# Kernel tuning notes

Measured on AMD Instinct MI355X. Metric: run time of the kernel, lower is better.

Reference implementation:

```python
import jax, jax.numpy as jnp
import numpy as np

N_EMBD = 2048
N_HEAD = 16
N_KV_HEAD = 4
HD = N_EMBD // N_HEAD  # 128
B, T = 1, 4096
EPS = 1e-6


def apply_rope(x, cos, sin):
    # x: [B,T,H,hd]; cos/sin: [T,1,hd//2]
    hd = x.shape[-1] // 2
    x1, x2 = x[..., :hd], x[..., hd:]
    y1 = x1 * cos + x2 * sin
    y2 = x2 * cos - x1 * sin
    return jnp.concatenate((y1, y2), axis=-1).astype(x.dtype)


def rms_norm(x, eps=EPS):
    return x * jax.lax.rsqrt(jnp.mean(jnp.square(x), axis=-1, keepdims=True) + eps)


def setup_inputs() -> dict:
    key = jax.random.key(0)
    ks = jax.random.split(key, 7)
    s = 0.02
    return {
        "x": jax.random.normal(ks[0], (B, T, N_EMBD), dtype=jnp.float32),
        "cos": jax.random.normal(ks[1], (T, 1, HD // 2), dtype=jnp.float32),
        "sin": jax.random.normal(ks[2], (T, 1, HD // 2), dtype=jnp.float32),
        "wq": jax.random.normal(ks[3], (N_EMBD, N_HEAD * HD), dtype=jnp.float32) * s,
        "wk": jax.random.normal(ks[4], (N_EMBD, N_KV_HEAD * HD), dtype=jnp.float32) * s,
        "wv": jax.random.normal(ks[5], (N_EMBD, N_KV_HEAD * HD), dtype=jnp.float32) * s,
        "wo": jax.random.normal(ks[6], (N_EMBD, N_EMBD), dtype=jnp.float32) * s,
    }


def reference(x, cos, sin, wq, wk, wv, wo):
    Bb, Tt, C = x.shape
    q = (x @ wq).reshape(Bb, Tt, N_HEAD, HD)
    k = (x @ wk).reshape(Bb, Tt, N_KV_HEAD, HD)
    v = (x @ wv).reshape(Bb, Tt, N_KV_HEAD, HD)
    q = rms_norm(apply_rope(q, cos, sin))
    k = rms_norm(apply_rope(k, cos, sin))
    g = N_HEAD // N_KV_HEAD
    if g > 1:
        k = jnp.repeat(k, g, axis=2)  # [B,T,H,hd]
        v = jnp.repeat(v, g, axis=2)
    scale = 1.0 / jnp.sqrt(jnp.float32(HD))
    # scores: [B,H,T,S]
    scores = jnp.einsum("bthd,bshd->bhts", q, k) * scale
    causal = jnp.tril(jnp.ones((Tt, Tt), dtype=bool))
    scores = jnp.where(causal, scores, jnp.finfo(scores.dtype).min)
    attn = jax.nn.softmax(scores, axis=-1)
    y = jnp.einsum("bhts,bshd->bthd", attn, v).reshape(Bb, Tt, C)
    return y @ wo
```

## Files before the change

### kernel.cpp

```cpp
#include <hip/hip_runtime.h>

#define T_SEQ 4096
#define C_EMB 2048
#define NH 16
#define NKV 4
#define HD 128

typedef short bf16x8 __attribute__((ext_vector_type(8)));
typedef float f32x4 __attribute__((ext_vector_type(4)));
typedef unsigned short u16x4 __attribute__((ext_vector_type(4)));

__device__ inline unsigned short f2bf(float f) {
    unsigned int u = __float_as_uint(f);
    unsigned int r = (u + 0x7FFFu + ((u >> 16) & 1u)) >> 16;
    return (unsigned short)r;
}

__device__ __forceinline__ void async_cp16(const unsigned short* g, unsigned short* l) {
    __builtin_amdgcn_global_load_lds((const __attribute__((address_space(1))) unsigned int*)g,
                                     (__attribute__((address_space(3))) unsigned int*)l,
                                     16, 0, 0);
}

__global__ __launch_bounds__(256) void cvt_bf16(const float* __restrict__ in,
                                                unsigned short* __restrict__ out, int n) {
    int i = (blockIdx.x * 256 + threadIdx.x) * 4;
    if (i >= n) return;
    float4 f = *(const float4*)(&in[i]);
    u16x4 o;
    o.x = f2bf(f.x); o.y = f2bf(f.y); o.z = f2bf(f.z); o.w = f2bf(f.w);
    *(u16x4*)(&out[i]) = o;
}

__global__ __launch_bounds__(256) void transpose_all(const float* __restrict__ wq,
                                                     const float* __restrict__ wk,
                                                     const float* __restrict__ wv,
                                                     const float* __restrict__ wo,
                                                     unsigned short* __restrict__ wqkvT,
                                                     unsigned short* __restrict__ woT) {
    __shared__ float tile[32][33];
    int z = blockIdx.z;
    const float* in;
    unsigned short* out;
    int ld_in;
    if (z == 0)      { in = wq; out = wqkvT;                         ld_in = 2048; }
    else if (z == 1) { in = wk; out = wqkvT + (size_t)2048 * 2048;   ld_in = 512;  }
    else if (z == 2) { in = wv; out = wqkvT + (size_t)2560 * 2048;   ld_in = 512;  }
    else             { in = wo; out = woT;                           ld_in = 2048; }
    if ((z == 1 || z == 2) && blockIdx.x >= 16) return;

    int x = blockIdx.x * 32 + threadIdx.x;
    for (int i = threadIdx.y; i < 32; i += 8) {
        int y = blockIdx.y * 32 + i;
        tile[i][threadIdx.x] = in[(size_t)y * ld_in + x];
    }
    __syncthreads();
    int xo = blockIdx.y * 32 + threadIdx.x;
    for (int i = threadIdx.y; i < 32; i += 8) {
        int yo = blockIdx.x * 32 + i;
        out[(size_t)yo * 2048 + xo] = f2bf(tile[threadIdx.x][i]);
    }
}

__global__ __launch_bounds__(256, 4) void gemm_qkv(const unsigned short* __restrict__ A,
                                                   const unsigned short* __restrict__ Bt,
                                                   const float* __restrict__ cosb,
                                                   const float* __restrict__ sinb,
                                                   unsigned short* __restrict__ Qn,
                                                   unsigned short* __restrict__ Kn,
                                                   unsigned short* __restrict__ Vt) {
    __shared__ __align__(16) unsigned short As[2][128 * 32];
    __shared__ __align__(16) unsigned short Bs[2][128 * 32];
    const int K = 2048;
    int t = threadIdx.x;
    int w = t >> 6, lane = t & 63;
    int ln = lane & 15, q = lane >> 4;
    int wm = w * 32;
    int m0 = blockIdx.y * 128, n0 = blockIdx.x * 128;

    f32x4 acc[2][8] = {};

#pragma unroll
    for (int s = 0; s < 2; ++s) {
        int L = s * 256 + t;
        int r = L >> 2;
        int c = (L & 3) ^ ((L >> 4) & 3);
        async_cp16(&A[(size_t)(m0 + r) * K + c * 8], &As[0][s * 2048 + w * 512]);
        async_cp16(&Bt[(size_t)(n0 + r) * K + c * 8], &Bs[0][s * 2048 + w * 512]);
    }

    for (int it = 0; it < 64; ++it) {
        __syncthreads();
        if (it < 63) {
            int k0 = (it + 1) * 32;
            int p = (it + 1) & 1;
#pragma unroll
            for (int s = 0; s < 2; ++s) {
                int L = s * 256 + t;
                int r = L >> 2;
                int c = (L & 3) ^ ((L >> 4) & 3);
                async_cp16(&A[(size_t)(m0 + r) * K + k0 + c * 8], &As[p][s * 2048 + w * 512]);
                async_cp16(&Bt[(size_t)(n0 + r) * K + k0 + c * 8], &Bs[p][s * 2048 + w * 512]);
            }
        }
        int p = it & 1;
        int cs = (q ^ ((ln >> 2) & 3)) * 8;
        bf16x8 af[2], bfr[8];
#pragma unroll
        for (int i = 0; i < 2; ++i) af[i] = *(const bf16x8*)(&As[p][(wm + i * 16 + ln) * 32 + cs]);
#pragma unroll
        for (int j = 0; j < 8; ++j) bfr[j] = *(const bf16x8*)(&Bs[p][(j * 16 + ln) * 32 + cs]);
#pragma unroll
        for (int i = 0; i < 2; ++i)
#pragma unroll
            for (int j = 0; j < 8; ++j)
                acc[i][j] = __builtin_amdgcn_mfma_f32_16x16x32_bf16(af[i], bfr[j], acc[i][j], 0, 0, 0);
    }

    if (n0 < 2560) {
        bool isQ = (n0 < 2048);
        int h = isQ ? (n0 >> 7) : ((n0 - 2048) >> 7);
#pragma unroll
        for (int i = 0; i < 2; ++i)
#pragma unroll
            for (int r = 0; r < 4; ++r) {
                int row = m0 + wm + i * 16 + q * 4 + r;
                float y1[4], y2[4];
                float ss = 0.0f;
#pragma unroll
                for (int j = 0; j < 4; ++j) {
                    float a = acc[i][j][r];
                    float b = acc[i][j + 4][r];
                    float cc = cosb[row * 64 + j * 16 + ln];
                    float sv = sinb[row * 64 + j * 16 + ln];
                    y1[j] = a * cc + b * sv;
                    y2[j] = b * cc - a * sv;
                    ss += y1[j] * y1[j] + y2[j] * y2[j];
                }
                ss += __shfl_xor(ss, 1);
                ss += __shfl_xor(ss, 2);
                ss += __shfl_xor(ss, 4);
                ss += __shfl_xor(ss, 8);
                float rv = rsqrtf(ss * (1.0f / 128.0f) + 1e-6f);
                if (isQ) {
                    float s = rv * (0.08838834764831845f * 1.4426950408889634f);
                    unsigned short* ob = Qn + (size_t)row * 2048 + h * 128;
#pragma unroll
                    for (int j = 0; j < 4; ++j) {
                        ob[j * 16 + ln] = f2bf(y1[j] * s);
                        ob[64 + j * 16 + ln] = f2bf(y2[j] * s);
                    }
                } else {
                    unsigned short* ob = Kn + (size_t)row * 512 + h * 128;
#pragma unroll
                    for (int j = 0; j < 4; ++j) {
                        ob[j * 16 + ln] = f2bf(y1[j] * rv);
                        ob[64 + j * 16 + ln] = f2bf(y2[j] * rv);
                    }
                }
            }
    } else {
        int v0 = n0 - 2560;
        unsigned short* sm = &As[0][0];
#pragma unroll
        for (int half = 0; half < 2; ++half) {
            __syncthreads();
#pragma unroll
            for (int i = 0; i < 2; ++i)
#pragma unroll
                for (int jj = 0; jj < 4; ++jj) {
                    int j = half * 4 + jj;
                    int cc = jj * 16 + ln;
                    int rr = wm + i * 16 + q * 4;
                    u16x4 pk;
                    pk.x = f2bf(acc[i][j][0]); pk.y = f2bf(acc[i][j][1]);
                    pk.z = f2bf(acc[i][j][2]); pk.w = f2bf(acc[i][j][3]);
                    *(u16x4*)(&sm[cc * 136 + rr]) = pk;
                }
            __syncthreads();
            int vtr = t >> 2, mseg = (t & 3) * 32;
            unsigned short* dst = Vt + (size_t)(v0 + half * 64 + vtr) * 4096 + m0 + mseg;
            const unsigned short* src = &sm[vtr * 136 + mseg];
            *(int4*)(dst)      = *(const int4*)(src);
            *(int4*)(dst + 8)  = *(const int4*)(src + 8);
            *(int4*)(dst + 16) = *(const int4*)(src + 16);
            *(int4*)(dst + 24) = *(const int4*)(src + 24);
        }
    }
}

__global__ __launch_bounds__(256, 4) void gemm_bt_db(const unsigned short* __restrict__ A,
                                                     const unsigned short* __restrict__ Bt,
                                                     float* __restrict__ C, int M, int N, int K) {
    __shared__ __align__(16) unsigned short As[2][128 * 32];
    __shared__ __align__(16) unsigned short Bs[2][128 * 32];
    int t = threadIdx.x;
    int w = t >> 6, lane = t & 63;
    int ln = lane & 15, q = lane >> 4;
    int wm = (w >> 1) * 64, wn = (w & 1) * 64;
    int m0 = blockIdx.y * 128, n0 = blockIdx.x * 128;

    f32x4 acc[4][4] = {};

#pragma unroll
    for (int s = 0; s < 2; ++s) {
        int L = s * 256 + t;
        int r = L >> 2;
        int c = (L & 3) ^ ((L >> 4) & 3);
        async_cp16(&A[(size_t)(m0 + r) * K + c * 8], &As[0][s * 2048 + w * 512]);
        async_cp16(&Bt[(size_t)(n0 + r) * K + c * 8], &Bs[0][s * 2048 + w * 512]);
    }

    int niter = K >> 5;
    for (int it = 0; it < niter; ++it) {
        __syncthreads();
        if (it < niter - 1) {
            int k0 = (it + 1) * 32;
            int p = (it + 1) & 1;
#pragma unroll
            for (int s = 0; s < 2; ++s) {
                int L = s * 256 + t;
                int r = L >> 2;
                int c = (L & 3) ^ ((L >> 4) & 3);
                async_cp16(&A[(size_t)(m0 + r) * K + k0 + c * 8], &As[p][s * 2048 + w * 512]);
                async_cp16(&Bt[(size_t)(n0 + r) * K + k0 + c * 8], &Bs[p][s * 2048 + w * 512]);
            }
        }
        int p = it & 1;
        int cs = (q ^ ((ln >> 2) & 3)) * 8;
        bf16x8 af[4], bfr[4];
#pragma unroll
        for (int i = 0; i < 4; ++i) af[i] = *(const bf16x8*)(&As[p][(wm + i * 16 + ln) * 32 + cs]);
#pragma unroll
        for (int j = 0; j < 4; ++j) bfr[j] = *(const bf16x8*)(&Bs[p][(wn + j * 16 + ln) * 32 + cs]);
#pragma unroll
        for (int i = 0; i < 4; ++i)
#pragma unroll
            for (int j = 0; j < 4; ++j)
                acc[i][j] = __builtin_amdgcn_mfma_f32_16x16x32_bf16(af[i], bfr[j], acc[i][j], 0, 0, 0);
    }
#pragma unroll
    for (int i = 0; i < 4; ++i)
#pragma unroll
        for (int j = 0; j < 4; ++j)
#pragma unroll
            for (int r = 0; r < 4; ++r) {
                int row = m0 + wm + i * 16 + q * 4 + r;
                int col = n0 + wn + j * 16 + ln;
                C[(size_t)row * N + col] = acc[i][j][r];
            }
}

__global__ __launch_bounds__(128) void flash_attn(const unsigned short* __restrict__ Qn,
                                                  const unsigned short* __restrict__ Kn,
                                                  const unsigned short* __restrict__ Vt,
                                                  unsigned short* __restrict__ Ao) {
    __shared__ __align__(16) unsigned short Ks[2][64 * 128];
    __shared__ __align__(16) unsigned short Vs[2][128 * 64];
    __shared__ __align__(16) unsigned short Pl[2][32 * 72];

    int pairi = blockIdx.x;
    int h = blockIdx.y;
    int kvh = h >> 2;
    int t = threadIdx.x;
    int w = t >> 6, lane = t & 63;
    int ln = lane & 15, q = lane >> 4;

    int nA = 64 - pairi;
    int bq = 63 - pairi;
    int wq0 = bq * 64 + w * 32;

    bf16x8 qf[2][4];
#pragma unroll
    for (int i = 0; i < 2; ++i) {
        const unsigned short* qb = Qn + (size_t)(wq0 + i * 16 + ln) * 2048 + h * 128;
#pragma unroll
        for (int kc = 0; kc < 4; ++kc) qf[i][kc] = *(const bf16x8*)(qb + kc * 32 + q * 8);
    }

    f32x4 o[2][8] = {};
    f32x4 l_p[2] = {};

#pragma unroll
    for (int s = 0; s < 8; ++s) {
        int L = s * 128 + t;
        int key = L >> 4;
        int c = (L & 15) ^ (key & 15);
        async_cp16(Kn + (size_t)key * 512 + kvh * 128 + c * 8, &Ks[0][s * 1024 + w * 512]);
    }
#pragma unroll
    for (int s = 0; s < 8; ++s) {
        int L = s * 128 + t;
        int hd = L >> 3;
        int c = (L & 7) ^ (hd & 7);
        async_cp16(Vt + (size_t)(kvh * 128 + hd) * 4096 + c * 8, &Vs[0][s * 1024 + w * 512]);
    }

    for (int it = 0; it < 65; ++it) {
        __syncthreads();

        int nxt = it + 1;
        if (nxt < 65) {
            int nkt = (nxt < nA) ? nxt * 64 : (nxt - nA) * 64;
            unsigned short* kd = Ks[nxt & 1];
            unsigned short* vd = Vs[nxt & 1];
#pragma unroll
            for (int s = 0; s < 8; ++s) {
                int L = s * 128 + t;
                int key = L >> 4;
                int c = (L & 15) ^ (key & 15);
                async_cp16(Kn + (size_t)(nkt + key) * 512 + kvh * 128 + c * 8,
                           kd + s * 1024 + w * 512);
            }
#pragma unroll
            for (int s = 0; s < 8; ++s) {
                int L = s * 128 + t;
                int hd = L >> 3;
                int c = (L & 7) ^ (hd & 7);
                async_cp16(Vt + (size_t)(kvh * 128 + hd) * 4096 + nkt + c * 8,
                           vd + s * 1024 + w * 512);
            }
        }

        if (it == nA) {
#pragma unroll
            for (int i = 0; i < 2; ++i)
#pragma unroll
                for (int r = 0; r < 4; ++r) {
                    float lsum = l_p[i][r];
                    lsum += __shfl_xor(lsum, 1);
                    lsum += __shfl_xor(lsum, 2);
                    lsum += __shfl_xor(lsum, 4);
                    lsum += __shfl_xor(lsum, 8);
                    float inv = 1.0f / lsum;
                    int row = wq0 + i * 16 + q * 4 + r;
                    unsigned short* ob = Ao + (size_t)row * 2048 + h * 128;
#pragma unroll
                    for (int f = 0; f < 8; ++f) ob[f * 16 + ln] = f2bf(o[i][f][r] * inv);
                }
            bq = pairi;
            wq0 = bq * 64 + w * 32;
#pragma unroll
            for (int i = 0; i < 2; ++i) {
                const unsigned short* qb = Qn + (size_t)(wq0 + i * 16 + ln) * 2048 + h * 128;
#pragma unroll
                for (int kc = 0; kc < 4; ++kc) qf[i][kc] = *(const bf16x8*)(qb + kc * 32 + q * 8);
            }
#pragma unroll
            for (int i = 0; i < 2; ++i) {
#pragma unroll
                for (int f = 0; f < 8; ++f) o[i][f] = (f32x4){0.f, 0.f, 0.f, 0.f};
                l_p[i] = (f32x4){0.f, 0.f, 0.f, 0.f};
            }
        }

        int kt0 = (it < nA) ? it * 64 : (it - nA) * 64;
        const unsigned short* kb = Ks[it & 1];
        const unsigned short* vb = Vs[it & 1];

        f32x4 sA[2][4];
#pragma unroll
        for (int i = 0; i < 2; ++i)
#pragma unroll
            for (int jt = 0; jt < 4; ++jt)
                sA[i][jt] = (f32x4){-16.6f, -16.6f, -16.6f, -16.6f};

#pragma unroll
        for (int jt = 0; jt < 4; ++jt) {
            int key = jt * 16 + ln;
#pragma unroll
            for (int kc = 0; kc < 4; ++kc) {
                int cs = ((kc * 4 + q) ^ ln) * 8;
                bf16x8 kf = *(const bf16x8*)(&kb[key * 128 + cs]);
                sA[0][jt] = __builtin_amdgcn_mfma_f32_16x16x32_bf16(qf[0][kc], kf, sA[0][jt], 0, 0, 0);
                sA[1][jt] = __builtin_amdgcn_mfma_f32_16x16x32_bf16(qf[1][kc], kf, sA[1][jt], 0, 0, 0);
            }
        }
        if (kt0 + 63 > wq0) {
#pragma unroll
            for (int i = 0; i < 2; ++i)
#pragma unroll
                for (int jt = 0; jt < 4; ++jt)
#pragma unroll
                    for (int r = 0; r < 4; ++r) {
                        int key = kt0 + jt * 16 + ln;
                        int row = wq0 + i * 16 + q * 4 + r;
                        if (key > row) sA[i][jt][r] = -3e38f;
                    }
        }
#pragma unroll
        for (int i = 0; i < 2; ++i)
#pragma unroll
            for (int r = 0; r < 4; ++r) {
                int prow = (i * 16 + q * 4 + r) * 72;
#pragma unroll
                for (int jt = 0; jt < 4; ++jt) {
                    float p = __builtin_amdgcn_exp2f(sA[i][jt][r]);
                    Pl[w][prow + jt * 16 + ln] = (unsigned short)(__float_as_uint(p) >> 16);
                    l_p[i][r] += p;
                }
            }

#pragma unroll
        for (int ks = 0; ks < 2; ++ks) {
            bf16x8 pa0 = *(const bf16x8*)(&Pl[w][ln * 72 + ks * 32 + q * 8]);
            bf16x8 pa1 = *(const bf16x8*)(&Pl[w][(16 + ln) * 72 + ks * 32 + q * 8]);
            int cs = ((ks * 4 + q) ^ (ln & 7)) * 8;
#pragma unroll
            for (int f = 0; f < 8; ++f) {
                bf16x8 vf = *(const bf16x8*)(&vb[(f * 16 + ln) * 64 + cs]);
                o[0][f] = __builtin_amdgcn_mfma_f32_16x16x32_bf16(pa0, vf, o[0][f], 0, 0, 0);
                o[1][f] = __builtin_amdgcn_mfma_f32_16x16x32_bf16(pa1, vf, o[1][f], 0, 0, 0);
            }
        }
    }
#pragma unroll
    for (int i = 0; i < 2; ++i)
#pragma unroll
        for (int r = 0; r < 4; ++r) {
            float lsum = l_p[i][r];
            lsum += __shfl_xor(lsum, 1);
            lsum += __shfl_xor(lsum, 2);
            lsum += __shfl_xor(lsum, 4);
            lsum += __shfl_xor(lsum, 8);
            float inv = 1.0f / lsum;
            int row = wq0 + i * 16 + q * 4 + r;
            unsigned short* ob = Ao + (size_t)row * 2048 + h * 128;
#pragma unroll
            for (int f = 0; f < 8; ++f) ob[f * 16 + ln] = f2bf(o[i][f][r] * inv);
        }
}

extern "C" void kernel_launch(void* const* d_in, const int* in_sizes, int n_in,
                              void* d_out, int out_size, void* d_ws, size_t ws_size,
                              hipStream_t stream) {
    const float* x    = (const float*)d_in[0];
    const float* cosb = (const float*)d_in[1];
    const float* sinb = (const float*)d_in[2];
    const float* wq   = (const float*)d_in[3];
    const float* wk   = (const float*)d_in[4];
    const float* wv   = (const float*)d_in[5];
    const float* wo   = (const float*)d_in[6];
    float* out = (float*)d_out;

    char* ws = (char*)d_ws;
    unsigned short* xb    = (unsigned short*)ws;
    unsigned short* wqkvT = xb    + (size_t)4096 * 2048;
    unsigned short* woT   = wqkvT + (size_t)3072 * 2048;
    unsigned short* Qn    = woT   + (size_t)2048 * 2048;
    unsigned short* Kn    = Qn    + (size_t)4096 * 2048;
    unsigned short* Vt    = Kn    + (size_t)4096 * 512;
    unsigned short* Ao    = Vt    + (size_t)512 * 4096;

    cvt_bf16<<<(4096 * 2048 / 4 + 255) / 256, 256, 0, stream>>>(x, xb, 4096 * 2048);
    transpose_all<<<dim3(64, 64, 4), dim3(32, 8), 0, stream>>>(wq, wk, wv, wo, wqkvT, woT);
    gemm_qkv<<<dim3(24, 32), 256, 0, stream>>>(xb, wqkvT, cosb, sinb, Qn, Kn, Vt);
    flash_attn<<<dim3(32, 16), 128, 0, stream>>>(Qn, Kn, Vt, Ao);
    gemm_bt_db<<<dim3(16, 32), 256, 0, stream>>>(Ao, woT, out, 4096, 2048, 2048);
}
```

Before: 399.0 us.

## Replace paired causal query blocks with one block per CTA and 32-key tiles

Drops the scheme where each CTA handled a complementary pair of query blocks (long plus short) to balance causal work. It now launches one CTA per 64-row query block, 1024 CTAs instead of 512, and iterates over 32-key tiles, which halves shared memory per CTA. The intent is more CTAs resident per CU and finer causal masking granularity. In exchange the per-CTA work becomes uneven and each tile costs relatively more in barriers and loads.

```diff
diff --git a/kernel.cpp b/kernel.cpp
--- a/kernel.cpp
+++ b/kernel.cpp
@@ -255,20 +255,19 @@
                                                   const unsigned short* __restrict__ Kn,
                                                   const unsigned short* __restrict__ Vt,
                                                   unsigned short* __restrict__ Ao) {
-    __shared__ __align__(16) unsigned short Ks[2][64 * 128];
-    __shared__ __align__(16) unsigned short Vs[2][128 * 64];
-    __shared__ __align__(16) unsigned short Pl[2][32 * 72];
-
-    int pairi = blockIdx.x;
+    __shared__ __align__(16) unsigned short Ks[2][32 * 128];
+    __shared__ __align__(16) unsigned short Vs[2][128 * 32];
+    __shared__ __align__(16) unsigned short Pl[2][32 * 40];
+
+    int bq = 63 - blockIdx.x;
     int h = blockIdx.y;
     int kvh = h >> 2;
     int t = threadIdx.x;
     int w = t >> 6, lane = t & 63;
     int ln = lane & 15, q = lane >> 4;
 
-    int nA = 64 - pairi;
-    int bq = 63 - pairi;
     int wq0 = bq * 64 + w * 32;
+    int niter = 2 * bq + 2;
 
     bf16x8 qf[2][4];
 #pragma unroll
@@ -282,30 +281,30 @@
     f32x4 l_p[2] = {};
 
 #pragma unroll
-    for (int s = 0; s < 8; ++s) {
+    for (int s = 0; s < 4; ++s) {
         int L = s * 128 + t;
         int key = L >> 4;
         int c = (L & 15) ^ (key & 15);
         async_cp16(Kn + (size_t)key * 512 + kvh * 128 + c * 8, &Ks[0][s * 1024 + w * 512]);
     }
 #pragma unroll
-    for (int s = 0; s < 8; ++s) {
+    for (int s = 0; s < 4; ++s) {
         int L = s * 128 + t;
-        int hd = L >> 3;
-        int c = (L & 7) ^ (hd & 7);
+        int hd = L >> 2;
+        int c = (L & 3) ^ (hd & 3);
         async_cp16(Vt + (size_t)(kvh * 128 + hd) * 4096 + c * 8, &Vs[0][s * 1024 + w * 512]);
     }
 
-    for (int it = 0; it < 65; ++it) {
+    for (int it = 0; it < niter; ++it) {
         __syncthreads();
 
         int nxt = it + 1;
-        if (nxt < 65) {
-            int nkt = (nxt < nA) ? nxt * 64 : (nxt - nA) * 64;
+        if (nxt < niter) {
+            int nkt = nxt * 32;
             unsigned short* kd = Ks[nxt & 1];
             unsigned short* vd = Vs[nxt & 1];
 #pragma unroll
-            for (int s = 0; s < 8; ++s) {
+            for (int s = 0; s < 4; ++s) {
                 int L = s * 128 + t;
                 int key = L >> 4;
                 int c = (L & 15) ^ (key & 15);
@@ -313,60 +312,28 @@
                            kd + s * 1024 + w * 512);
             }
 #pragma unroll
-            for (int s = 0; s < 8; ++s) {
+            for (int s = 0; s < 4; ++s) {
                 int L = s * 128 + t;
-                int hd = L >> 3;
-                int c = (L & 7) ^ (hd & 7);
+                int hd = L >> 2;
+                int c = (L & 3) ^ (hd & 3);
                 async_cp16(Vt + (size_t)(kvh * 128 + hd) * 4096 + nkt + c * 8,
                            vd + s * 1024 + w * 512);
             }
         }
 
-        if (it == nA) {
-#pragma unroll
-            for (int i = 0; i < 2; ++i)
-#pragma unroll
-                for (int r = 0; r < 4; ++r) {
-                    float lsum = l_p[i][r];
-                    lsum += __shfl_xor(lsum, 1);
-                    lsum += __shfl_xor(lsum, 2);
-                    lsum += __shfl_xor(lsum, 4);
-                    lsum += __shfl_xor(lsum, 8);
-                    float inv = 1.0f / lsum;
-                    int row = wq0 + i * 16 + q * 4 + r;
-                    unsigned short* ob = Ao + (size_t)row * 2048 + h * 128;
-#pragma unroll
-                    for (int f = 0; f < 8; ++f) ob[f * 16 + ln] = f2bf(o[i][f][r] * inv);
-                }
-            bq = pairi;
-            wq0 = bq * 64 + w * 32;
-#pragma unroll
-            for (int i = 0; i < 2; ++i) {
-                const unsigned short* qb = Qn + (size_t)(wq0 + i * 16 + ln) * 2048 + h * 128;
-#pragma unroll
-                for (int kc = 0; kc < 4; ++kc) qf[i][kc] = *(const bf16x8*)(qb + kc * 32 + q * 8);
-            }
-#pragma unroll
-            for (int i = 0; i < 2; ++i) {
-#pragma unroll
-                for (int f = 0; f < 8; ++f) o[i][f] = (f32x4){0.f, 0.f, 0.f, 0.f};
-                l_p[i] = (f32x4){0.f, 0.f, 0.f, 0.f};
-            }
-        }
-
-        int kt0 = (it < nA) ? it * 64 : (it - nA) * 64;
+        int kt0 = it * 32;
         const unsigned short* kb = Ks[it & 1];
         const unsigned short* vb = Vs[it & 1];
 
-        f32x4 sA[2][4];
+        f32x4 sA[2][2];
 #pragma unroll
         for (int i = 0; i < 2; ++i)
 #pragma unroll
-            for (int jt = 0; jt < 4; ++jt)
+            for (int jt = 0; jt < 2; ++jt)
                 sA[i][jt] = (f32x4){-16.6f, -16.6f, -16.6f, -16.6f};
 
 #pragma unroll
-        for (int jt = 0; jt < 4; ++jt) {
+        for (int jt = 0; jt < 2; ++jt) {
             int key = jt * 16 + ln;
 #pragma unroll
             for (int kc = 0; kc < 4; ++kc) {
@@ -376,11 +343,11 @@
                 sA[1][jt] = __builtin_amdgcn_mfma_f32_16x16x32_bf16(qf[1][kc], kf, sA[1][jt], 0, 0, 0);
             }
         }
-        if (kt0 + 63 > wq0) {
+        if (kt0 + 31 > wq0) {
 #pragma unroll
             for (int i = 0; i < 2; ++i)
 #pragma unroll
-                for (int jt = 0; jt < 4; ++jt)
+                for (int jt = 0; jt < 2; ++jt)
 #pragma unroll
                     for (int r = 0; r < 4; ++r) {
                         int key = kt0 + jt * 16 + ln;
@@ -392,28 +359,26 @@
         for (int i = 0; i < 2; ++i)
 #pragma unroll
             for (int r = 0; r < 4; ++r) {
-                int prow = (i * 16 + q * 4 + r) * 72;
-#pragma unroll
-                for (int jt = 0; jt < 4; ++jt) {
+                int prow = (i * 16 + q * 4 + r) * 40;
+#pragma unroll
+                for (int jt = 0; jt < 2; ++jt) {
                     float p = __builtin_amdgcn_exp2f(sA[i][jt][r]);
                     Pl[w][prow + jt * 16 + ln] = (unsigned short)(__float_as_uint(p) >> 16);
                     l_p[i][r] += p;
                 }
             }
 
-#pragma unroll
-        for (int ks = 0; ks < 2; ++ks) {
-            bf16x8 pa0 = *(const bf16x8*)(&Pl[w][ln * 72 + ks * 32 + q * 8]);
-            bf16x8 pa1 = *(const bf16x8*)(&Pl[w][(16 + ln) * 72 + ks * 32 + q * 8]);
-            int cs = ((ks * 4 + q) ^ (ln & 7)) * 8;
-#pragma unroll
-            for (int f = 0; f < 8; ++f) {
-                bf16x8 vf = *(const bf16x8*)(&vb[(f * 16 + ln) * 64 + cs]);
-                o[0][f] = __builtin_amdgcn_mfma_f32_16x16x32_bf16(pa0, vf, o[0][f], 0, 0, 0);
-                o[1][f] = __builtin_amdgcn_mfma_f32_16x16x32_bf16(pa1, vf, o[1][f], 0, 0, 0);
-            }
-        }
-    }
+        bf16x8 pa0 = *(const bf16x8*)(&Pl[w][ln * 40 + q * 8]);
+        bf16x8 pa1 = *(const bf16x8*)(&Pl[w][(16 + ln) * 40 + q * 8]);
+        int cs = (q ^ (ln & 3)) * 8;
+#pragma unroll
+        for (int f = 0; f < 8; ++f) {
+            bf16x8 vf = *(const bf16x8*)(&vb[(f * 16 + ln) * 32 + cs]);
+            o[0][f] = __builtin_amdgcn_mfma_f32_16x16x32_bf16(pa0, vf, o[0][f], 0, 0, 0);
+            o[1][f] = __builtin_amdgcn_mfma_f32_16x16x32_bf16(pa1, vf, o[1][f], 0, 0, 0);
+        }
+    }
+
 #pragma unroll
     for (int i = 0; i < 2; ++i)
 #pragma unroll
@@ -455,6 +420,6 @@
     cvt_bf16<<<(4096 * 2048 / 4 + 255) / 256, 256, 0, stream>>>(x, xb, 4096 * 2048);
     transpose_all<<<dim3(64, 64, 4), dim3(32, 8), 0, stream>>>(wq, wk, wv, wo, wqkvT, woT);
     gemm_qkv<<<dim3(24, 32), 256, 0, stream>>>(xb, wqkvT, cosb, sinb, Qn, Kn, Vt);
-    flash_attn<<<dim3(32, 16), 128, 0, stream>>>(Qn, Kn, Vt, Ao);
+    flash_attn<<<dim3(64, 16), 128, 0, stream>>>(Qn, Kn, Vt, Ao);
     gemm_bt_db<<<dim3(16, 32), 256, 0, stream>>>(Ao, woT, out, 4096, 2048, 2048);
 }
```

Result: slower. 429.6 us (+7.7%).
